# Kernel optimization log

Measured on AMD Instinct MI355X. Metric: run time of the kernel, lower is better.

The kernel has to match this reference:

```python
import jax, jax.numpy as jnp
import numpy as np

B, S, E, D = 32, 2048, 1024, 1024


def setup_inputs() -> dict:
    key = jax.random.key(0)
    k0, k1, k2, k3, k4 = jax.random.split(key, 5)
    scale_e = 1.0 / np.sqrt(E)
    scale_d = 1.0 / np.sqrt(D)
    return {
        "hidden": jax.random.normal(k0, (B, D), dtype=jnp.float32),
        "encoder_outputs": jax.random.normal(k1, (S, B, E), dtype=jnp.float32),
        "We": jax.random.normal(k2, (D, E), dtype=jnp.float32) * scale_e,
        "Wd": jax.random.normal(k3, (D, D), dtype=jnp.float32) * scale_d,
        "v": jax.random.normal(k4, (D,), dtype=jnp.float32) * scale_d,
    }


def reference(hidden, encoder_outputs, We, Wd, v):
    # encoder projection: [S,B,E] x [D,E] -> [B,S,D] (batch-first for the add)
    enc_proj = jnp.einsum("sbe,de->bsd", encoder_outputs, We)
    # decoder projection broadcast over src positions: [B,1,D]
    dec_proj = (hidden @ Wd.T)[:, None, :]
    energy = jnp.tanh(enc_proj + dec_proj)          # [B,S,D]
    scores = jnp.einsum("bsd,d->bs", energy, v)     # v-layer, squeeze(-1)
    attention_weights = jax.nn.softmax(scores, axis=1)  # softmax over src_len
    # weighted sum of encoder outputs: bmm([B,1,S],[B,S,E]) -> [B,E]
    context = jnp.einsum("bs,sbe->be", attention_weights, encoder_outputs)
    return context, attention_weights
```

## Files before the change

### kernel.cpp

```cpp
#include <hip/hip_runtime.h>
#include <cmath>
#include <cstdint>

constexpr int B_ = 32;
constexpr int S_ = 2048;
constexpr int E_ = 1024;
constexpr int D_ = 1024;
constexpr int K_ = E_;
constexpr int M_ = S_ * B_;
constexpr int SC_ = 32;
constexpr int NP_ = 16;

typedef float f32x4 __attribute__((ext_vector_type(4)));
typedef float fvec4 __attribute__((ext_vector_type(4)));
typedef __bf16 bf16x8 __attribute__((ext_vector_type(8)));
typedef __attribute__((address_space(3))) uint32_t lds_u32;
typedef const __attribute__((address_space(1))) uint32_t g_u32;

__device__ __forceinline__ float fast_tanh(float x) {
    float e = __builtin_amdgcn_exp2f(x * 2.88539008177793f);
    return 1.f - 2.f * __builtin_amdgcn_rcpf(e + 1.f);
}

__device__ __forceinline__ uint16_t f2bf(float f) {
    uint32_t u = __float_as_uint(f);
    u += 0x7FFFu + ((u >> 16) & 1u);
    return (uint16_t)(u >> 16);
}

constexpr int ENC_N8 = M_ * K_ / 8;
constexpr int WE_N8  = D_ * K_ / 8;
constexpr int CVT_BLOCKS = (ENC_N8 + WE_N8) / 256;
constexpr int DEC_BLOCKS = (B_ * D_) / 4;

__global__ __launch_bounds__(256) void prep_kernel(
    const float* __restrict__ enc, uint16_t* __restrict__ encb,
    const float* __restrict__ We,  uint16_t* __restrict__ Web,
    const float* __restrict__ hidden, const float* __restrict__ Wd,
    float* __restrict__ dec)
{
    const int bid = blockIdx.x;
    if (bid < CVT_BLOCKS) {
        int tid = bid * 256 + threadIdx.x;
        const float* src;
        uint16_t* dst;
        int i8;
        if (tid < ENC_N8) { src = enc; dst = encb; i8 = tid; }
        else              { src = We;  dst = Web;  i8 = tid - ENC_N8; }
        const fvec4* s4 = reinterpret_cast<const fvec4*>(src) + (size_t)i8 * 2;
        fvec4 a = __builtin_nontemporal_load(s4);
        fvec4 b = __builtin_nontemporal_load(s4 + 1);
        uint4 o;
        o.x = (uint32_t)f2bf(a.x) | ((uint32_t)f2bf(a.y) << 16);
        o.y = (uint32_t)f2bf(a.z) | ((uint32_t)f2bf(a.w) << 16);
        o.z = (uint32_t)f2bf(b.x) | ((uint32_t)f2bf(b.y) << 16);
        o.w = (uint32_t)f2bf(b.z) | ((uint32_t)f2bf(b.w) << 16);
        reinterpret_cast<uint4*>(dst)[i8] = o;
    } else {
        const int o = (bid - CVT_BLOCKS) * 4 + (threadIdx.x >> 6);
        const int lane = threadIdx.x & 63;
        const int b = o >> 10;
        const int d = o & (D_ - 1);
        const float4* h4 = reinterpret_cast<const float4*>(hidden + (size_t)b * D_);
        const float4* w4 = reinterpret_cast<const float4*>(Wd + (size_t)d * D_);
        float acc = 0.f;
#pragma unroll
        for (int p = 0; p < 4; ++p) {
            float4 h = h4[lane + p * 64], w = w4[lane + p * 64];
            acc += h.x * w.x + h.y * w.y + h.z * w.z + h.w * w.w;
        }
#pragma unroll
        for (int off = 32; off > 0; off >>= 1) acc += __shfl_xor(acc, off);
        if (lane == 0) dec[o] = acc;
    }
}

constexpr int TM2 = 256, TN2 = 256, TK2 = 32;
constexpr int NT2 = K_ / TK2;
constexpr int TILE_B = TM2 * TK2 * 2;
constexpr int BUF_B  = TILE_B * 2;

#define TILE_STEP(T, DO_STAGE)                                                \
  do {                                                                        \
    const int buf_ = (T) & 3;                                                 \
    const char* bufA_ = ldsc + buf_ * BUF_B;                                  \
    const char* bufB_ = bufA_ + TILE_B;                                       \
    bf16x8 a0_[4], bv_[4];                                                    \
    _Pragma("unroll")                                                         \
    for (int i = 0; i < 4; ++i)                                               \
      a0_[i] = __builtin_bit_cast(bf16x8,                                     \
          *reinterpret_cast<const int4*>(bufA_ + offA[i]));                   \
    _Pragma("unroll")                                                         \
    for (int j = 0; j < 4; ++j)                                               \
      bv_[j] = __builtin_bit_cast(bf16x8,                                     \
          *reinterpret_cast<const int4*>(bufB_ + offB[j]));                   \
    if (DO_STAGE) {                                                           \
      char* sb_ = ldsc + (((T) + 3) & 3) * BUF_B;                             \
      __builtin_amdgcn_global_load_lds((g_u32*)pA0, (lds_u32*)(sb_ + dst0), 16, 0, 0); \
      __builtin_amdgcn_global_load_lds((g_u32*)pA1, (lds_u32*)(sb_ + dst1), 16, 0, 0); \
      pA0 += TK2; pA1 += TK2;                                                 \
    }                                                                         \
    asm volatile("s_waitcnt lgkmcnt(0)" ::: "memory");                        \
    __builtin_amdgcn_sched_barrier(0);                                        \
    __builtin_amdgcn_s_setprio(1);                                            \
    _Pragma("unroll")                                                         \
    for (int i = 0; i < 4; ++i)                                               \
      _Pragma("unroll")                                                       \
      for (int j = 0; j < 4; ++j)                                             \
        acc[i][j] = __builtin_amdgcn_mfma_f32_16x16x32_bf16(                  \
            a0_[i], bv_[j], acc[i][j], 0, 0, 0);                              \
    __builtin_amdgcn_s_setprio(0);                                            \
    bf16x8 a1_[4];                                                            \
    _Pragma("unroll")                                                         \
    for (int i = 0; i < 4; ++i)                                               \
      a1_[i] = __builtin_bit_cast(bf16x8,                                     \
          *reinterpret_cast<const int4*>(bufA_ + offA[4 + i]));               \
    if (DO_STAGE) {                                                           \
      char* sb_ = ldsc + (((T) + 3) & 3) * BUF_B + TILE_B;                    \
      __builtin_amdgcn_global_load_lds((g_u32*)pB0, (lds_u32*)(sb_ + dst0), 16, 0, 0); \
      __builtin_amdgcn_global_load_lds((g_u32*)pB1, (lds_u32*)(sb_ + dst1), 16, 0, 0); \
      pB0 += TK2; pB1 += TK2;                                                 \
    }                                                                         \
    asm volatile("s_waitcnt lgkmcnt(0)" ::: "memory");                        \
    __builtin_amdgcn_sched_barrier(0);                                        \
    __builtin_amdgcn_s_setprio(1);                                            \
    _Pragma("unroll")                                                         \
    for (int i = 0; i < 4; ++i)                                               \
      _Pragma("unroll")                                                       \
      for (int j = 0; j < 4; ++j)                                             \
        acc[4 + i][j] = __builtin_amdgcn_mfma_f32_16x16x32_bf16(              \
            a1_[i], bv_[j], acc[4 + i][j], 0, 0, 0);                          \
    __builtin_amdgcn_s_setprio(0);                                            \
  } while (0)

__global__ __launch_bounds__(512, 2) void score_mfma_kernel(
    const uint16_t* __restrict__ A,
    const uint16_t* __restrict__ Bw,
    const float* __restrict__ dec,
    const float* __restrict__ v,
    float* __restrict__ spart)
{
    __shared__ __align__(16) uint16_t smem[4 * 2 * TM2 * TK2];

    const int p    = blockIdx.x;
    const int xcd  = p & 7;
    const int slot = p >> 3;
    const int nb   = slot & 3;
    const int mb   = xcd + 8 * (slot >> 2);
    const int m0 = mb * TM2;
    const int n0 = nb * TN2;

    const int tid  = threadIdx.x;
    const int wave = tid >> 6;
    const int lane = tid & 63;
    const int wm   = wave >> 2;
    const int wn   = wave & 3;
    const int q    = lane >> 4;
    const int r16  = lane & 15;

    char* ldsc = (char*)smem;

    int offA[8], offB[4];
#pragma unroll
    for (int i = 0; i < 8; ++i) {
        const int r = wm * 128 + i * 16 + r16;
        offA[i] = (r * 64 + q * 16) ^ ((r & 7) << 4);
    }
#pragma unroll
    for (int j = 0; j < 4; ++j) {
        const int r = wn * 64 + j * 16 + r16;
        offB[j] = (r * 64 + q * 16) ^ ((r & 7) << 4);
    }

    const int l2     = lane >> 2;
    const int bbit   = (lane >> 4) & 1;
    const int rowSwz = l2 ^ bbit;
    const int gsel   = (lane & 3) ^ (rowSwz & 3);
    const uint16_t* pA0 = A  + (size_t)(m0 + wave * 32 +  0 + rowSwz) * K_ + gsel * 8;
    const uint16_t* pA1 = A  + (size_t)(m0 + wave * 32 + 16 + rowSwz) * K_ + gsel * 8;
    const uint16_t* pB0 = Bw + (size_t)(n0 + wave * 32 +  0 + rowSwz) * K_ + gsel * 8;
    const uint16_t* pB1 = Bw + (size_t)(n0 + wave * 32 + 16 + rowSwz) * K_ + gsel * 8;
    const int dst0 = wave * 2048;
    const int dst1 = dst0 + 1024;

#pragma unroll
    for (int tt = 0; tt < 3; ++tt) {
        char* sb = ldsc + tt * BUF_B;
        __builtin_amdgcn_global_load_lds((g_u32*)pA0, (lds_u32*)(sb + dst0), 16, 0, 0);
        __builtin_amdgcn_global_load_lds((g_u32*)pA1, (lds_u32*)(sb + dst1), 16, 0, 0);
        __builtin_amdgcn_global_load_lds((g_u32*)pB0, (lds_u32*)(sb + TILE_B + dst0), 16, 0, 0);
        __builtin_amdgcn_global_load_lds((g_u32*)pB1, (lds_u32*)(sb + TILE_B + dst1), 16, 0, 0);
        pA0 += TK2; pA1 += TK2; pB0 += TK2; pB1 += TK2;
    }
    asm volatile("s_waitcnt vmcnt(8)" ::: "memory");
    __builtin_amdgcn_s_barrier();

    f32x4 acc[8][4] = {};

#pragma unroll 1
    for (int t = 0; t < NT2 - 3; ++t) {
        TILE_STEP(t, true);
        asm volatile("s_waitcnt vmcnt(8)" ::: "memory");
        __builtin_amdgcn_s_barrier();
    }
    TILE_STEP(NT2 - 3, false);
    asm volatile("s_waitcnt vmcnt(4)" ::: "memory");
    __builtin_amdgcn_s_barrier();
    TILE_STEP(NT2 - 2, false);
    asm volatile("s_waitcnt vmcnt(0)" ::: "memory");
    __builtin_amdgcn_s_barrier();
    TILE_STEP(NT2 - 1, false);

    float vj[4];
#pragma unroll
    for (int j = 0; j < 4; ++j) vj[j] = v[n0 + wn * 64 + j * 16 + r16];
    float dec_r[2][4][4];
#pragma unroll
    for (int i01 = 0; i01 < 2; ++i01)
#pragma unroll
        for (int r = 0; r < 4; ++r) {
            const int b = i01 * 16 + q * 4 + r;
#pragma unroll
            for (int j = 0; j < 4; ++j)
                dec_r[i01][r][j] = dec[b * D_ + n0 + wn * 64 + j * 16 + r16];
        }

    float* plane = spart + (size_t)(nb * 4 + wn) * M_;

#pragma unroll
    for (int i = 0; i < 8; ++i) {
#pragma unroll
        for (int r = 0; r < 4; ++r) {
            const int m = m0 + wm * 128 + i * 16 + q * 4 + r;
            const int b = (i & 1) * 16 + q * 4 + r;
            float pv = 0.f;
#pragma unroll
            for (int j = 0; j < 4; ++j)
                pv += vj[j] * fast_tanh(acc[i][j][r] + dec_r[i & 1][r][j]);
            pv += __shfl_xor(pv, 1);
            pv += __shfl_xor(pv, 2);
            pv += __shfl_xor(pv, 4);
            pv += __shfl_xor(pv, 8);
            if (r16 == 0) plane[b * S_ + (m >> 5)] = pv;
        }
    }
}

__global__ __launch_bounds__(256) void softmax16_kernel(
    const float* __restrict__ spart,
    float* __restrict__ attn)
{
    const int b = blockIdx.x;
    const int t = threadIdx.x;
    __shared__ float sm[256];

    const float4* base = reinterpret_cast<const float4*>(spart + (size_t)b * S_);
    constexpr int PSTRIDE = M_ / 4;
    float4 v0 = {0, 0, 0, 0}, v1 = {0, 0, 0, 0};
#pragma unroll
    for (int p = 0; p < NP_; ++p) {
        float4 a = base[(size_t)p * PSTRIDE + t];
        float4 c = base[(size_t)p * PSTRIDE + t + 256];
        v0.x += a.x; v0.y += a.y; v0.z += a.z; v0.w += a.w;
        v1.x += c.x; v1.y += c.y; v1.z += c.z; v1.w += c.w;
    }

    float lmax = fmaxf(fmaxf(fmaxf(v0.x, v0.y), fmaxf(v0.z, v0.w)),
                       fmaxf(fmaxf(v1.x, v1.y), fmaxf(v1.z, v1.w)));
    sm[t] = lmax; __syncthreads();
    for (int off = 128; off > 0; off >>= 1) {
        if (t < off) sm[t] = fmaxf(sm[t], sm[t + off]);
        __syncthreads();
    }
    const float mx = sm[0];
    __syncthreads();

    v0.x = __builtin_amdgcn_exp2f((v0.x - mx) * 1.44269504f);
    v0.y = __builtin_amdgcn_exp2f((v0.y - mx) * 1.44269504f);
    v0.z = __builtin_amdgcn_exp2f((v0.z - mx) * 1.44269504f);
    v0.w = __builtin_amdgcn_exp2f((v0.w - mx) * 1.44269504f);
    v1.x = __builtin_amdgcn_exp2f((v1.x - mx) * 1.44269504f);
    v1.y = __builtin_amdgcn_exp2f((v1.y - mx) * 1.44269504f);
    v1.z = __builtin_amdgcn_exp2f((v1.z - mx) * 1.44269504f);
    v1.w = __builtin_amdgcn_exp2f((v1.w - mx) * 1.44269504f);

    float lsum = v0.x + v0.y + v0.z + v0.w + v1.x + v1.y + v1.z + v1.w;
    sm[t] = lsum; __syncthreads();
    for (int off = 128; off > 0; off >>= 1) {
        if (t < off) sm[t] += sm[t + off];
        __syncthreads();
    }
    const float inv = 1.f / sm[0];
    float4* op = reinterpret_cast<float4*>(attn + (size_t)b * S_);
    v0.x *= inv; v0.y *= inv; v0.z *= inv; v0.w *= inv;
    v1.x *= inv; v1.y *= inv; v1.z *= inv; v1.w *= inv;
    op[t] = v0; op[t + 256] = v1;
}

__global__ __launch_bounds__(256) void context_part_kernel(
    const uint16_t* __restrict__ encb, const float* __restrict__ attn,
    float* __restrict__ part)
{
    const int b  = blockIdx.x & (B_ - 1);
    const int sc = blockIdx.x >> 5;
    const int e0 = threadIdx.x * 4;
    constexpr int SLEN = S_ / SC_;

    float a0 = 0.f, a1 = 0.f, a2 = 0.f, a3 = 0.f;
    const int s0 = sc * SLEN;
#pragma unroll 2
    for (int s = s0; s < s0 + SLEN; ++s) {
        const float w = attn[b * S_ + s];
        uint2 u = *reinterpret_cast<const uint2*>(
            encb + ((size_t)s * B_ + b) * E_ + e0);
        a0 += w * __uint_as_float((u.x & 0xFFFFu) << 16);
        a1 += w * __uint_as_float(u.x & 0xFFFF0000u);
        a2 += w * __uint_as_float((u.y & 0xFFFFu) << 16);
        a3 += w * __uint_as_float(u.y & 0xFFFF0000u);
    }
    float4 o = {a0, a1, a2, a3};
    *reinterpret_cast<float4*>(part + ((size_t)sc * B_ + b) * E_ + e0) = o;
}

__global__ __launch_bounds__(256) void context_reduce_kernel(
    const float* __restrict__ part, float* __restrict__ ctx)
{
    const int i = blockIdx.x * 256 + threadIdx.x;
    float acc = 0.f;
#pragma unroll
    for (int sc = 0; sc < SC_; ++sc) acc += part[(size_t)sc * B_ * E_ + i];
    ctx[i] = acc;
}

constexpr int BM = 64, BN = 64, BK = 16;

__global__ __launch_bounds__(256) void dec_proj_wave_kernel(
    const float* __restrict__ hidden, const float* __restrict__ Wd,
    float* __restrict__ dec)
{
    const int o = blockIdx.x * 4 + (threadIdx.x >> 6);
    const int lane = threadIdx.x & 63;
    const int b = o >> 10;
    const int d = o & (D_ - 1);
    const float4* h4 = reinterpret_cast<const float4*>(hidden + (size_t)b * D_);
    const float4* w4 = reinterpret_cast<const float4*>(Wd + (size_t)d * D_);
    float acc = 0.f;
#pragma unroll
    for (int p = 0; p < 4; ++p) {
        float4 h = h4[lane + p * 64], w = w4[lane + p * 64];
        acc += h.x * w.x + h.y * w.y + h.z * w.z + h.w * w.w;
    }
#pragma unroll
    for (int off = 32; off > 0; off >>= 1) acc += __shfl_xor(acc, off);
    if (lane == 0) dec[o] = acc;
}

__global__ __launch_bounds__(256) void score_gemm_kernel(
    const float* __restrict__ enc, const float* __restrict__ We,
    const float* __restrict__ dec, const float* __restrict__ v,
    float* __restrict__ scores)
{
    __shared__ float As[BM][BK + 1];
    __shared__ float Bs[BN][BK + 1];
    __shared__ float red[BM][17];
    const int m0 = blockIdx.x * BM;
    const int n0 = blockIdx.y * BN;
    const int t  = threadIdx.x;
    const int tx = t & 15;
    const int ty = t >> 4;
    const int lrow = t >> 2;
    const int lcol = (t & 3) * 4;
    float acc[4][4] = {};
    for (int k0 = 0; k0 < E_; k0 += BK) {
        float4 a = *reinterpret_cast<const float4*>(enc + (size_t)(m0 + lrow) * E_ + k0 + lcol);
        float4 w = *reinterpret_cast<const float4*>(We + (size_t)(n0 + lrow) * E_ + k0 + lcol);
        As[lrow][lcol + 0] = a.x; As[lrow][lcol + 1] = a.y;
        As[lrow][lcol + 2] = a.z; As[lrow][lcol + 3] = a.w;
        Bs[lrow][lcol + 0] = w.x; Bs[lrow][lcol + 1] = w.y;
        Bs[lrow][lcol + 2] = w.z; Bs[lrow][lcol + 3] = w.w;
        __syncthreads();
#pragma unroll
        for (int kk = 0; kk < BK; ++kk) {
            float av[4], bw[4];
#pragma unroll
            for (int i = 0; i < 4; ++i) av[i] = As[ty * 4 + i][kk];
#pragma unroll
            for (int j = 0; j < 4; ++j) bw[j] = Bs[tx * 4 + j][kk];
#pragma unroll
            for (int i = 0; i < 4; ++i)
#pragma unroll
                for (int j = 0; j < 4; ++j)
                    acc[i][j] += av[i] * bw[j];
        }
        __syncthreads();
    }
    float pp[4];
#pragma unroll
    for (int i = 0; i < 4; ++i) {
        int m = m0 + ty * 4 + i;
        int b = m & (B_ - 1);
        float s = 0.f;
#pragma unroll
        for (int j = 0; j < 4; ++j) {
            int n = n0 + tx * 4 + j;
            s += v[n] * tanhf(acc[i][j] + dec[b * D_ + n]);
        }
        pp[i] = s;
    }
#pragma unroll
    for (int i = 0; i < 4; ++i) red[ty * 4 + i][tx] = pp[i];
    __syncthreads();
    if (t < BM) {
        float s = 0.f;
#pragma unroll
        for (int j = 0; j < 16; ++j) s += red[t][j];
        atomicAdd(&scores[m0 + t], s);
    }
}

__global__ __launch_bounds__(256) void softmax_kernel(
    const float* __restrict__ scores, float* __restrict__ attn)
{
    const int b = blockIdx.x;
    const int t = threadIdx.x;
    __shared__ float sm[256];
    float vals[8];
    float lmax = -INFINITY;
#pragma unroll
    for (int i = 0; i < 8; ++i) {
        int s = t + i * 256;
        vals[i] = scores[s * B_ + b];
        lmax = fmaxf(lmax, vals[i]);
    }
    sm[t] = lmax; __syncthreads();
    for (int off = 128; off > 0; off >>= 1) {
        if (t < off) sm[t] = fmaxf(sm[t], sm[t + off]);
        __syncthreads();
    }
    const float mx = sm[0];
    __syncthreads();
    float lsum = 0.f;
#pragma unroll
    for (int i = 0; i < 8; ++i) {
        vals[i] = expf(vals[i] - mx);
        lsum += vals[i];
    }
    sm[t] = lsum; __syncthreads();
    for (int off = 128; off > 0; off >>= 1) {
        if (t < off) sm[t] += sm[t + off];
        __syncthreads();
    }
    const float inv = 1.f / sm[0];
#pragma unroll
    for (int i = 0; i < 8; ++i)
        attn[b * S_ + t + i * 256] = vals[i] * inv;
}

__global__ __launch_bounds__(256) void context_kernel(
    const float* __restrict__ enc, const float* __restrict__ attn,
    float* __restrict__ ctx)
{
    const int e0 = (blockIdx.x & 3) * 256;
    const int b  = (blockIdx.x >> 2) & (B_ - 1);
    const int sc = blockIdx.x >> 7;
    const int e  = e0 + threadIdx.x;
    float acc = 0.f;
    const int s_end = sc * 256 + 256;
    for (int s = sc * 256; s < s_end; ++s)
        acc += attn[b * S_ + s] * enc[((size_t)s * B_ + b) * E_ + e];
    atomicAdd(&ctx[b * E_ + e], acc);
}

extern "C" void kernel_launch(void* const* d_in, const int* in_sizes, int n_in,
                              void* d_out, int out_size, void* d_ws, size_t ws_size,
                              hipStream_t stream) {
    const float* hidden = (const float*)d_in[0];
    const float* enc    = (const float*)d_in[1];
    const float* We     = (const float*)d_in[2];
    const float* Wd     = (const float*)d_in[3];
    const float* v      = (const float*)d_in[4];

    float* ctx  = (float*)d_out;
    float* attn = (float*)d_out + B_ * E_;

    float*    dec   = (float*)d_ws;
    float*    spart = dec + B_ * D_;
    uint16_t* Web   = (uint16_t*)(spart + (size_t)NP_ * M_);
    uint16_t* encb  = Web + (size_t)D_ * K_;

    const size_t need = (size_t)B_ * D_ * 4 + (size_t)NP_ * M_ * 4
                      + ((size_t)D_ * K_ + (size_t)M_ * K_) * 2;
    const bool fast = ws_size >= need;

    if (fast) {
        prep_kernel<<<CVT_BLOCKS + DEC_BLOCKS, 256, 0, stream>>>(
            enc, encb, We, Web, hidden, Wd, dec);

        score_mfma_kernel<<<(M_ / TM2) * (D_ / TN2), 512, 0, stream>>>(
            encb, Web, dec, v, spart);

        softmax16_kernel<<<B_, 256, 0, stream>>>(spart, attn);
        context_part_kernel<<<SC_ * B_, 256, 0, stream>>>(encb, attn, spart);
        context_reduce_kernel<<<(B_ * E_) / 256, 256, 0, stream>>>(spart, ctx);
    } else {
        float* scores = spart;
        hipMemsetAsync(scores, 0, (size_t)M_ * sizeof(float), stream);
        hipMemsetAsync(ctx, 0, (size_t)B_ * E_ * sizeof(float), stream);
        dec_proj_wave_kernel<<<(B_ * D_) / 4, 256, 0, stream>>>(hidden, Wd, dec);
        dim3 g2(M_ / BM, D_ / BN);
        score_gemm_kernel<<<g2, 256, 0, stream>>>(enc, We, dec, v, scores);
        softmax_kernel<<<B_, 256, 0, stream>>>(scores, attn);
        context_kernel<<<B_ * 4 * 8, 256, 0, stream>>>(enc, attn, ctx);
    }
}
```

Before: 538.9 us.

## Software-pipeline LDS fragment reads one tile ahead in score GEMM

Restructures the MFMA main loop so the A and B fragments for tile t+1 are read from LDS during tile t, using ping-pong register sets, and removes the explicit lgkmcnt waits between LDS reads and MFMAs. The wait depth on global-to-LDS loads drops from vmcnt(8) to vmcnt(4) so the next buffer is ready before the early read. The goal is to hide LDS read latency behind MFMA work. In exchange it uses more registers under launch bounds of 512 threads with 2 blocks, and leaves less slack for the global loads.

Result: no change. 529.0 us (-1.8%).

```diff
diff --git a/kernel.cpp b/kernel.cpp
--- a/kernel.cpp
+++ b/kernel.cpp
@@ -80,27 +80,29 @@
 constexpr int TILE_B = TM2 * TK2 * 2;
 constexpr int BUF_B  = TILE_B * 2;
 
-#define TILE_STEP(T, DO_STAGE)                                                \
+#define STAGE_A(T)                                                            \
+  do { char* sb_ = ldsc + (((T) + 3) & 3) * BUF_B;                            \
+    __builtin_amdgcn_global_load_lds((g_u32*)pA0, (lds_u32*)(sb_ + dst0), 16, 0, 0); \
+    __builtin_amdgcn_global_load_lds((g_u32*)pA1, (lds_u32*)(sb_ + dst1), 16, 0, 0); \
+    pA0 += TK2; pA1 += TK2; } while (0)
+
+#define STAGE_B(T)                                                            \
+  do { char* sb_ = ldsc + (((T) + 3) & 3) * BUF_B + TILE_B;                   \
+    __builtin_amdgcn_global_load_lds((g_u32*)pB0, (lds_u32*)(sb_ + dst0), 16, 0, 0); \
+    __builtin_amdgcn_global_load_lds((g_u32*)pB1, (lds_u32*)(sb_ + dst1), 16, 0, 0); \
+    pB0 += TK2; pB1 += TK2; } while (0)
+
+#define TILE_PIPE(T, DO_STAGE, aC, bC, aN, bN)                                \
   do {                                                                        \
-    const int buf_ = (T) & 3;                                                 \
-    const char* bufA_ = ldsc + buf_ * BUF_B;                                  \
-    const char* bufB_ = bufA_ + TILE_B;                                       \
-    bf16x8 a0_[4], bv_[4];                                                    \
-    _Pragma("unroll")                                                         \
-    for (int i = 0; i < 4; ++i)                                               \
-      a0_[i] = __builtin_bit_cast(bf16x8,                                     \
-          *reinterpret_cast<const int4*>(bufA_ + offA[i]));                   \
-    _Pragma("unroll")                                                         \
-    for (int j = 0; j < 4; ++j)                                               \
-      bv_[j] = __builtin_bit_cast(bf16x8,                                     \
-          *reinterpret_cast<const int4*>(bufB_ + offB[j]));                   \
-    if (DO_STAGE) {                                                           \
-      char* sb_ = ldsc + (((T) + 3) & 3) * BUF_B;                             \
-      __builtin_amdgcn_global_load_lds((g_u32*)pA0, (lds_u32*)(sb_ + dst0), 16, 0, 0); \
-      __builtin_amdgcn_global_load_lds((g_u32*)pA1, (lds_u32*)(sb_ + dst1), 16, 0, 0); \
-      pA0 += TK2; pA1 += TK2;                                                 \
-    }                                                                         \
-    asm volatile("s_waitcnt lgkmcnt(0)" ::: "memory");                        \
+    const char* bufA_  = ldsc + ((T) & 3) * BUF_B;                            \
+    const char* bufAn_ = ldsc + (((T) + 1) & 3) * BUF_B;                      \
+    const char* bufBn_ = bufAn_ + TILE_B;                                     \
+    bf16x8 a1_[4];                                                            \
+    _Pragma("unroll")                                                         \
+    for (int i = 0; i < 4; ++i)                                               \
+      a1_[i] = __builtin_bit_cast(bf16x8,                                     \
+          *reinterpret_cast<const int4*>(bufA_ + offA[4 + i]));               \
+    if (DO_STAGE) STAGE_A(T);                                                 \
     __builtin_amdgcn_sched_barrier(0);                                        \
     __builtin_amdgcn_s_setprio(1);                                            \
     _Pragma("unroll")                                                         \
@@ -108,20 +110,18 @@
       _Pragma("unroll")                                                       \
       for (int j = 0; j < 4; ++j)                                             \
         acc[i][j] = __builtin_amdgcn_mfma_f32_16x16x32_bf16(                  \
-            a0_[i], bv_[j], acc[i][j], 0, 0, 0);                              \
+            aC[i], bC[j], acc[i][j], 0, 0, 0);                                \
     __builtin_amdgcn_s_setprio(0);                                            \
-    bf16x8 a1_[4];                                                            \
-    _Pragma("unroll")                                                         \
-    for (int i = 0; i < 4; ++i)                                               \
-      a1_[i] = __builtin_bit_cast(bf16x8,                                     \
-          *reinterpret_cast<const int4*>(bufA_ + offA[4 + i]));               \
-    if (DO_STAGE) {                                                           \
-      char* sb_ = ldsc + (((T) + 3) & 3) * BUF_B + TILE_B;                    \
-      __builtin_amdgcn_global_load_lds((g_u32*)pB0, (lds_u32*)(sb_ + dst0), 16, 0, 0); \
-      __builtin_amdgcn_global_load_lds((g_u32*)pB1, (lds_u32*)(sb_ + dst1), 16, 0, 0); \
-      pB0 += TK2; pB1 += TK2;                                                 \
-    }                                                                         \
-    asm volatile("s_waitcnt lgkmcnt(0)" ::: "memory");                        \
+    __builtin_amdgcn_sched_barrier(0);                                        \
+    _Pragma("unroll")                                                         \
+    for (int i = 0; i < 4; ++i)                                               \
+      aN[i] = __builtin_bit_cast(bf16x8,                                      \
+          *reinterpret_cast<const int4*>(bufAn_ + offA[i]));                  \
+    _Pragma("unroll")                                                         \
+    for (int j = 0; j < 4; ++j)                                               \
+      bN[j] = __builtin_bit_cast(bf16x8,                                      \
+          *reinterpret_cast<const int4*>(bufBn_ + offB[j]));                  \
+    if (DO_STAGE) STAGE_B(T);                                                 \
     __builtin_amdgcn_sched_barrier(0);                                        \
     __builtin_amdgcn_s_setprio(1);                                            \
     _Pragma("unroll")                                                         \
@@ -129,9 +129,38 @@
       _Pragma("unroll")                                                       \
       for (int j = 0; j < 4; ++j)                                             \
         acc[4 + i][j] = __builtin_amdgcn_mfma_f32_16x16x32_bf16(              \
-            a1_[i], bv_[j], acc[4 + i][j], 0, 0, 0);                          \
+            a1_[i], bC[j], acc[4 + i][j], 0, 0, 0);                           \
     __builtin_amdgcn_s_setprio(0);                                            \
   } while (0)
+
+#define TILE_LAST(T, aC, bC)                                                  \
+  do {                                                                        \
+    const char* bufA_ = ldsc + ((T) & 3) * BUF_B;                             \
+    bf16x8 a1_[4];                                                            \
+    _Pragma("unroll")                                                         \
+    for (int i = 0; i < 4; ++i)                                               \
+      a1_[i] = __builtin_bit_cast(bf16x8,                                     \
+          *reinterpret_cast<const int4*>(bufA_ + offA[4 + i]));               \
+    __builtin_amdgcn_s_setprio(1);                                            \
+    _Pragma("unroll")                                                         \
+    for (int i = 0; i < 4; ++i)                                               \
+      _Pragma("unroll")                                                       \
+      for (int j = 0; j < 4; ++j)                                             \
+        acc[i][j] = __builtin_amdgcn_mfma_f32_16x16x32_bf16(                  \
+            aC[i], bC[j], acc[i][j], 0, 0, 0);                                \
+    _Pragma("unroll")                                                         \
+    for (int i = 0; i < 4; ++i)                                               \
+      _Pragma("unroll")                                                       \
+      for (int j = 0; j < 4; ++j)                                             \
+        acc[4 + i][j] = __builtin_amdgcn_mfma_f32_16x16x32_bf16(              \
+            a1_[i], bC[j], acc[4 + i][j], 0, 0, 0);                           \
+    __builtin_amdgcn_s_setprio(0);                                            \
+  } while (0)
+
+#define SYNC_VM4() do { asm volatile("s_waitcnt vmcnt(4)" ::: "memory");      \
+                        __builtin_amdgcn_s_barrier(); } while (0)
+#define SYNC_VM0() do { asm volatile("s_waitcnt vmcnt(0)" ::: "memory");      \
+                        __builtin_amdgcn_s_barrier(); } while (0)
 
 __global__ __launch_bounds__(512, 2) void score_mfma_kernel(
     const uint16_t* __restrict__ A,
@@ -192,24 +221,36 @@
         __builtin_amdgcn_global_load_lds((g_u32*)pB1, (lds_u32*)(sb + TILE_B + dst1), 16, 0, 0);
         pA0 += TK2; pA1 += TK2; pB0 += TK2; pB1 += TK2;
     }
-    asm volatile("s_waitcnt vmcnt(8)" ::: "memory");
-    __builtin_amdgcn_s_barrier();
-
-    f32x4 acc[8][4] = {};
-
-#pragma unroll 1
-    for (int t = 0; t < NT2 - 3; ++t) {
-        TILE_STEP(t, true);
-        asm volatile("s_waitcnt vmcnt(8)" ::: "memory");
-        __builtin_amdgcn_s_barrier();
-    }
-    TILE_STEP(NT2 - 3, false);
     asm volatile("s_waitcnt vmcnt(4)" ::: "memory");
     __builtin_amdgcn_s_barrier();
-    TILE_STEP(NT2 - 2, false);
-    asm volatile("s_waitcnt vmcnt(0)" ::: "memory");
+
+    f32x4 acc[8][4] = {};
+
+    bf16x8 aA[4], bA[4], aB[4], bB[4];
+#pragma unroll
+    for (int i = 0; i < 4; ++i)
+        aA[i] = __builtin_bit_cast(bf16x8,
+            *reinterpret_cast<const int4*>(ldsc + offA[i]));
+#pragma unroll
+    for (int j = 0; j < 4; ++j)
+        bA[j] = __builtin_bit_cast(bf16x8,
+            *reinterpret_cast<const int4*>(ldsc + TILE_B + offB[j]));
+
+#pragma unroll 2
+    for (int tp = 0; tp < 14; ++tp) {
+        const int t = tp * 2;
+        TILE_PIPE(t,     true, aA, bA, aB, bB);
+        SYNC_VM4();
+        TILE_PIPE(t + 1, true, aB, bB, aA, bA);
+        SYNC_VM4();
+    }
+    TILE_PIPE(28, true,  aA, bA, aB, bB);
+    SYNC_VM4();
+    TILE_PIPE(29, false, aB, bB, aA, bA);
+    SYNC_VM0();
+    TILE_PIPE(30, false, aA, bA, aB, bB);
     __builtin_amdgcn_s_barrier();
-    TILE_STEP(NT2 - 1, false);
+    TILE_LAST(31, aB, bB);
 
     float vj[4];
 #pragma unroll
```
